# Performance work log

Hardware: AMD Instinct MI355X
Metric: run time of the kernel (lower is better)

Reference implementation:

```python
import jax, jax.numpy as jnp
import numpy as np

E = 1024
H = 16
D = E // H  # head dim 64
B = 2
S = 2048


def setup_inputs() -> dict:
    key = jax.random.key(0)
    k1, k2, k3, k4, k5 = jax.random.split(key, 5)
    scale = 1.0 / np.sqrt(E)
    return {
        "x": jax.random.normal(k1, (B, S, E), dtype=jnp.float32),
        "W_in": jax.random.normal(k2, (E, 3 * E), dtype=jnp.float32) * scale,
        "b_in": jnp.zeros((3 * E,), dtype=jnp.float32),
        "W_out": jax.random.normal(k3, (E, E), dtype=jnp.float32) * scale,
        "b_out": jnp.zeros((E,), dtype=jnp.float32),
        "causal_mask": 1,
    }


def reference(x, W_in, b_in, W_out, b_out, causal_mask):
    b, s, e = x.shape
    qkv = x @ W_in + b_in                      # [B,S,3E]
    q, k, v = jnp.split(qkv, 3, axis=-1)
    # [B,S,E] -> [B,H,S,D]
    q = q.reshape(b, s, H, D).transpose(0, 2, 1, 3)
    k = k.reshape(b, s, H, D).transpose(0, 2, 1, 3)
    v = v.reshape(b, s, H, D).transpose(0, 2, 1, 3)
    scores = jnp.einsum("bhqd,bhkd->bhqk", q, k)
    if causal_mask:
        # mask applied before scaling in the original; -inf is scale-invariant
        mask = jnp.triu(jnp.ones((s, s), dtype=bool), k=1)
        scores = jnp.where(mask, -jnp.inf, scores)
    scores = scores / np.sqrt(D)
    weight = jax.nn.softmax(scores, axis=-1)
    out = jnp.einsum("bhqk,bhkd->bhqd", weight, v)   # [B,H,S,D]
    out = out.transpose(0, 2, 1, 3).reshape(b, s, e)
    return out @ W_out + b_out
```

## Files before the change

### kernel.cpp

```cpp
#include <hip/hip_runtime.h>
#include <hip/hip_bf16.h>
#include <cmath>

typedef __bf16 bf16;
typedef __attribute__((ext_vector_type(8))) __bf16 bf16x8;
typedef __attribute__((ext_vector_type(4))) __bf16 bf16x4;
typedef __attribute__((ext_vector_type(4))) float f32x4;
typedef __attribute__((ext_vector_type(16))) float f32x16;
typedef unsigned int u32;

constexpr int S  = 2048;
constexpr int E  = 1024;
constexpr int H  = 16;
constexpr int D  = 64;
constexpr int B  = 2;
constexpr int M  = B * S;
constexpr int N3 = 3 * E;
constexpr int NROWS = B * H * S;

__constant__ int P_tab_d[16] = {1,1,1,1,1,2,2,2,2,2,2,3,3,3,3,3};
__constant__ int S_tab_d[16] = {0,1,2,3,4,5,7,9,11,13,15,17,20,23,26,29};
__constant__ int c_ord_d[32] = {15,15,10,10, 15,14,14,14,13,9,9,4,
                                13,13,12,12,8,8, 12,11,11,11,7,7,3,
                                6,6, 5,5,2, 1, 0};
__constant__ int p_ord_d[32] = {1,2,0,1, 0,0,1,2,2,0,1,0,
                                0,1,1,2,0,1, 0,0,1,2,0,1,0,
                                0,1, 0,1,0, 0, 0};

static __device__ __forceinline__ void gload16(const void* g, void* l) {
  __builtin_amdgcn_global_load_lds((const __attribute__((address_space(1))) void*)g,
                                   (__attribute__((address_space(3))) void*)l, 16, 0, 0);
}

static __device__ __forceinline__ u32 pack2(float a, float b) {
  union { bf16 h[2]; u32 u; } r;
  r.h[0] = (bf16)a; r.h[1] = (bf16)b;
  return r.u;
}
typedef union { u32 w[4]; bf16x8 v; } FU;

__global__ void k_cvt(const float* __restrict__ in, bf16* __restrict__ out) {
  const int i = (blockIdx.x * blockDim.x + threadIdx.x) * 4;
  const float4 v = *(const float4*)(in + i);
  bf16x4 o = { (bf16)v.x, (bf16)v.y, (bf16)v.z, (bf16)v.w };
  *(bf16x4*)(out + i) = o;
}

__global__ void k_transpose_cvt(const float* __restrict__ in, bf16* __restrict__ out,
                                int R, int C) {
  __shared__ float t[32][33];
  const int c0 = blockIdx.x * 32, r0 = blockIdx.y * 32;
  const int tx = threadIdx.x, ty = threadIdx.y;
  #pragma unroll
  for (int j = 0; j < 32; j += 8)
    t[ty + j][tx] = in[(size_t)(r0 + ty + j) * C + c0 + tx];
  __syncthreads();
  #pragma unroll
  for (int j = 0; j < 32; j += 8)
    out[(size_t)(c0 + ty + j) * R + r0 + tx] = (bf16)t[tx][ty + j];
}

template<int EPI>
__global__ __launch_bounds__(256) void k_gemm(
    const bf16* __restrict__ A, const bf16* __restrict__ Bt,
    const float* __restrict__ bias, float* __restrict__ outF,
    bf16* __restrict__ oQ, bf16* __restrict__ oK, bf16* __restrict__ oV,
    int Kdim, int Nn)
{
  __shared__ __align__(16) char smem[65536];
  const int tid = threadIdx.x;
  const int lane = tid & 63, w = tid >> 6;
  const int lane15 = lane & 15, quad = lane >> 4;
  const int wm = w >> 1, wn = w & 1;

  const int nbx = Nn >> 7;
  const int nwg = gridDim.x;
  const int bid = blockIdx.x;
  const int swz = (bid & 7) * (nwg >> 3) + (bid >> 3);
  const int bn0 = (swz % nbx) * 128;
  const int bm0 = (swz / nbx) * 128;

  const int so0 = w * 1024 + lane * 16;
  int srow[4], slk[4];
  #pragma unroll
  for (int p = 0; p < 4; ++p) {
    const int o = p * 4096 + so0;
    const int row = o >> 7, cbyte = o & 127;
    srow[p] = row;
    slk[p] = (cbyte ^ ((row & 7) << 4)) >> 1;
  }

  f32x4 acc[4][4] = {};
  const int nkt = Kdim >> 6;

  #pragma unroll
  for (int p = 0; p < 4; ++p) {
    gload16(A  + (size_t)(bm0 + srow[p]) * Kdim + slk[p], smem +         p * 4096 + w * 1024);
    gload16(Bt + (size_t)(bn0 + srow[p]) * Kdim + slk[p], smem + 32768 + p * 4096 + w * 1024);
  }

  #pragma unroll 1
  for (int kt = 0; kt < nkt; ++kt) {
    const int cur = kt & 1;
    __builtin_amdgcn_s_barrier();
    if (kt + 1 < nkt) {
      const int k0 = (kt + 1) << 6;
      const int nb = (cur ^ 1) * 16384;
      #pragma unroll
      for (int p = 0; p < 4; ++p) {
        gload16(A  + (size_t)(bm0 + srow[p]) * Kdim + k0 + slk[p],
                smem + nb +         p * 4096 + w * 1024);
        gload16(Bt + (size_t)(bn0 + srow[p]) * Kdim + k0 + slk[p],
                smem + nb + 32768 + p * 4096 + w * 1024);
      }
      asm volatile("s_waitcnt vmcnt(8)" ::: "memory");
    } else {
      asm volatile("s_waitcnt vmcnt(0)" ::: "memory");
    }
    __builtin_amdgcn_s_barrier();

    const char* cA = smem + cur * 16384;
    const char* cB = smem + 32768 + cur * 16384;
    #pragma unroll
    for (int kk = 0; kk < 2; ++kk) {
      bf16x8 af[4], bfr[4];
      #pragma unroll
      for (int f = 0; f < 4; ++f) {
        const int ra = wm * 64 + f * 16 + lane15;
        af[f] = *(const bf16x8*)(cA + ra * 128 +
                 ((kk * 64 + (quad << 4)) ^ ((ra & 7) << 4)));
        const int rb = wn * 64 + f * 16 + lane15;
        bfr[f] = *(const bf16x8*)(cB + rb * 128 +
                 ((kk * 64 + (quad << 4)) ^ ((rb & 7) << 4)));
      }
      #pragma unroll
      for (int i = 0; i < 4; ++i)
        #pragma unroll
        for (int j = 0; j < 4; ++j)
          acc[i][j] = __builtin_amdgcn_mfma_f32_16x16x32_bf16(af[i], bfr[j], acc[i][j], 0, 0, 0);
    }
  }

  if constexpr (EPI == 1) {
    #pragma unroll
    for (int i = 0; i < 4; ++i)
      #pragma unroll
      for (int j = 0; j < 4; ++j) {
        const int n = bn0 + wn * 64 + j * 16 + lane15;
        const float bv = bias[n];
        #pragma unroll
        for (int r = 0; r < 4; ++r) {
          const int m = bm0 + wm * 64 + i * 16 + quad * 4 + r;
          outF[(size_t)m * E + n] = acc[i][j][r] + bv;
        }
      }
  } else {
    const int which = bn0 >> 10;
    const int b  = bm0 >> 11;
    const int s0 = bm0 & (S - 1);
    const int cn0 = bn0 & (E - 1);
    if (which < 2) {
      __builtin_amdgcn_s_barrier();
      char* lC = smem;
      #pragma unroll
      for (int j = 0; j < 4; ++j) {
        const int n_loc = wn * 64 + j * 16 + lane15;
        const float bv = bias[bn0 + n_loc];
        #pragma unroll
        for (int i = 0; i < 4; ++i)
          #pragma unroll
          for (int r = 0; r < 4; ++r) {
            const int m_loc = wm * 64 + i * 16 + quad * 4 + r;
            *(bf16*)(lC + m_loc * 256 + ((n_loc * 2) ^ ((m_loc & 7) << 4))) =
                (bf16)(acc[i][j][r] + bv);
          }
      }
      __builtin_amdgcn_s_barrier();
      const int h0 = cn0 >> 6;
      #pragma unroll
      for (int it = 0; it < 8; ++it) {
        const int cch = w * 64 + it * 8 + (lane >> 3);
        const int m_loc = cch >> 1, hh = cch & 1, piece = lane & 7;
        const bf16x8 vv = *(const bf16x8*)(lC + m_loc * 256 +
                          ((hh * 128 + piece * 16) ^ ((m_loc & 7) << 4)));
        if (which == 0) {
          *(bf16x8*)(oQ + ((size_t)(b * H + h0 + hh) * S + s0 + m_loc) * D + piece * 8) = vv;
        } else {
          const size_t hb = (size_t)(b * H + h0 + hh) * S * D;
          const int tile = (s0 + m_loc) >> 6;
          const int row = m_loc & 63;
          *(bf16x8*)(oK + hb + (size_t)tile * 4096 + (piece >> 1) * 1024 +
                     (row >> 5) * 512 + (32 * (piece & 1) + (row & 31)) * 8) = vv;
        }
      }
    } else {
      #pragma unroll
      for (int j = 0; j < 4; ++j) {
        const int n_loc = wn * 64 + j * 16 + lane15;
        const int cn = cn0 + n_loc;
        const int hv = cn >> 6, dd = cn & 63;
        const float bv = bias[bn0 + n_loc];
        const size_t hb = (size_t)(b * H + hv) * S * D;
        #pragma unroll
        for (int i = 0; i < 4; ++i) {
          const int scol_g = s0 + wm * 64 + i * 16 + quad * 4;
          const int vtile = scol_g >> 6;
          const int cg = (scol_g & 63) >> 3;
          bf16x4 pk = { (bf16)(acc[i][j][0] + bv), (bf16)(acc[i][j][1] + bv),
                        (bf16)(acc[i][j][2] + bv), (bf16)(acc[i][j][3] + bv) };
          *(bf16x4*)(oV + hb + (size_t)vtile * 4096 + (cg >> 1) * 1024 +
                     (dd >> 5) * 512 + (32 * (cg & 1) + (dd & 31)) * 8 +
                     (quad & 1) * 4) = pk;
        }
      }
    }
  }
}

__global__ __launch_bounds__(256, 4) void k_attn(
    const bf16* __restrict__ Qb, const bf16* __restrict__ Kf, const bf16* __restrict__ Vf,
    bf16* __restrict__ pO0, bf16* __restrict__ pO1,
    float* __restrict__ pM, float* __restrict__ pL, const int* __restrict__ cmask)
{
  __shared__ float corr_lds[4][32];
  __shared__ float lrow_lds[4][32];

  const int tid = threadIdx.x, lane = tid & 63, w = tid >> 6;
  const int h = lane >> 5, q31 = lane & 31;
  const int bh = blockIdx.x;
  const int yy = blockIdx.y;
  const int c  = c_ord_d[yy];
  const int p  = p_ord_d[yy];
  const int Pc = P_tab_d[c];
  const int sslot = S_tab_d[c] + p;
  const int causal = cmask[0];
  const float S2 = 0.18033688011112042f;

  const bf16* Qh = Qb + (size_t)bh * S * D;
  const bf16* Kh = Kf + (size_t)bh * S * D;
  const bf16* Vh = Vf + (size_t)bh * S * D;

  const int nt = causal ? (2 * c + 2) : (S / 64);
  const int t0 = (p * nt) / Pc;
  const int t1 = ((p + 1) * nt) / Pc;
  const int q0w = c * 128 + 32 * w;
  const int qg  = q0w + q31;
  const int t1w = causal ? min(t1, ((q0w + 31) >> 6) + 1) : t1;

  bf16x8 qf[4];
  #pragma unroll
  for (int ds = 0; ds < 4; ++ds)
    qf[ds] = *(const bf16x8*)(Qh + (size_t)qg * D + 16 * ds + 8 * h);

  f32x16 o0 = {}, o1 = {};
  float mrun = -INFINITY, lr = 0.f;

  #pragma unroll 1
  for (int t = t0; t < t1w; ++t) {
    const bf16* ktb = Kh + (size_t)t * 4096;
    const bf16* vtb = Vh + (size_t)t * 4096;

    bf16x8 kf0[4], kf1[4];
    #pragma unroll
    for (int ds = 0; ds < 4; ++ds) {
      kf0[ds] = *(const bf16x8*)(ktb + ds * 1024 +       lane * 8);
      kf1[ds] = *(const bf16x8*)(ktb + ds * 1024 + 512 + lane * 8);
    }

    f32x16 s0v = {}, s1v = {};
    __builtin_amdgcn_s_setprio(1);
    #pragma unroll
    for (int ds = 0; ds < 4; ++ds) {
      s0v = __builtin_amdgcn_mfma_f32_32x32x16_bf16(kf0[ds], qf[ds], s0v, 0, 0, 0);
      s1v = __builtin_amdgcn_mfma_f32_32x32x16_bf16(kf1[ds], qf[ds], s1v, 0, 0, 0);
    }
    __builtin_amdgcn_s_setprio(0);

    if (causal && (64 * t + 63 > q0w)) {
      #pragma unroll
      for (int rr = 0; rr < 16; ++rr) {
        const int kg = 64 * t + (rr & 3) + 8 * (rr >> 2) + 4 * h;
        if (kg > qg)      s0v[rr] = -INFINITY;
        if (kg + 32 > qg) s1v[rr] = -INFINITY;
      }
    }

    float a8[8];
    #pragma unroll
    for (int i = 0; i < 8; ++i)
      a8[i] = fmaxf(fmaxf(s0v[i], s0v[i + 8]), fmaxf(s1v[i], s1v[i + 8]));
    float tmax = fmaxf(fmaxf(fmaxf(a8[0], a8[1]), fmaxf(a8[2], a8[3])),
                       fmaxf(fmaxf(a8[4], a8[5]), fmaxf(a8[6], a8[7])));
    tmax = fmaxf(tmax, __shfl_xor(tmax, 32, 64));

    const bool nogrow = __all(tmax <= mrun);
    const float mnew = nogrow ? mrun : fmaxf(mrun, tmax);
    float corrf = 1.f;
    if (!nogrow) {
      corrf = __builtin_amdgcn_exp2f((mrun - mnew) * S2);
      corr_lds[w][q31] = corrf;
    }
    const float msc = mnew * S2;

    #pragma unroll
    for (int rr = 0; rr < 16; ++rr) {
      s0v[rr] = __builtin_amdgcn_exp2f(__builtin_fmaf(s0v[rr], S2, -msc));
      s1v[rr] = __builtin_amdgcn_exp2f(__builtin_fmaf(s1v[rr], S2, -msc));
    }

    float b8[8];
    #pragma unroll
    for (int i = 0; i < 8; ++i)
      b8[i] = (s0v[i] + s0v[i + 8]) + (s1v[i] + s1v[i + 8]);
    float psum = ((b8[0] + b8[1]) + (b8[2] + b8[3])) + ((b8[4] + b8[5]) + (b8[6] + b8[7]));
    psum += __shfl_xor(psum, 32, 64);
    lr = lr * corrf + psum;
    mrun = mnew;

    u32 pk[8][2];
    #pragma unroll
    for (int jj = 0; jj < 4; ++jj) {
      pk[jj][0]     = pack2(s0v[4 * jj],     s0v[4 * jj + 1]);
      pk[jj][1]     = pack2(s0v[4 * jj + 2], s0v[4 * jj + 3]);
      pk[jj + 4][0] = pack2(s1v[4 * jj],     s1v[4 * jj + 1]);
      pk[jj + 4][1] = pack2(s1v[4 * jj + 2], s1v[4 * jj + 3]);
    }

    if (!nogrow) {
      #pragma unroll
      for (int j = 0; j < 4; ++j) {
        const f32x4 cv = *(const f32x4*)&corr_lds[w][8 * j + 4 * h];
        #pragma unroll
        for (int sr = 0; sr < 4; ++sr) {
          o0[4 * j + sr] *= cv[sr];
          o1[4 * j + sr] *= cv[sr];
        }
      }
    }

    __builtin_amdgcn_s_setprio(1);
    #pragma unroll
    for (int ks = 0; ks < 4; ++ks) {
      u32 a0 = pk[2 * ks][0], b0 = pk[2 * ks + 1][0];
      u32 a1 = pk[2 * ks][1], b1 = pk[2 * ks + 1][1];
      asm volatile("v_permlane32_swap_b32 %0, %1" : "+v"(a0), "+v"(b0));
      asm volatile("v_permlane32_swap_b32 %0, %1" : "+v"(a1), "+v"(b1));
      FU f; f.w[0] = a0; f.w[1] = a1; f.w[2] = b0; f.w[3] = b1;
      const bf16x8 vf0 = *(const bf16x8*)(vtb + ks * 1024 +       lane * 8);
      const bf16x8 vf1 = *(const bf16x8*)(vtb + ks * 1024 + 512 + lane * 8);
      o0 = __builtin_amdgcn_mfma_f32_32x32x16_bf16(f.v, vf0, o0, 0, 0, 0);
      o1 = __builtin_amdgcn_mfma_f32_32x32x16_bf16(f.v, vf1, o1, 0, 0, 0);
    }
    __builtin_amdgcn_s_setprio(0);
  }

  const int slotbase = ((bh & 15) * 32 + sslot) * 128;
  if (h == 0) {
    pM[(size_t)(bh * 32 + sslot) * 128 + 32 * w + q31] = mrun;
    pL[(size_t)(bh * 32 + sslot) * 128 + 32 * w + q31] = lr;
  }
  lrow_lds[w][q31] = lr;
  bf16* po = (bh < 16 ? pO0 : pO1) + (size_t)slotbase * D;
  #pragma unroll
  for (int j = 0; j < 4; ++j) {
    const f32x4 lv = *(const f32x4*)&lrow_lds[w][8 * j + 4 * h];
    #pragma unroll
    for (int sr = 0; sr < 4; ++sr) {
      const int rr = 4 * j + sr;
      const float inv = lv[sr] > 0.f ? 1.0f / lv[sr] : 0.f;
      const int qloc = 32 * w + (rr & 3) + 8 * (rr >> 2) + 4 * h;
      bf16* dst = po + (size_t)qloc * D;
      dst[q31]      = (bf16)(o0[rr] * inv);
      dst[32 + q31] = (bf16)(o1[rr] * inv);
    }
  }
}

__global__ __launch_bounds__(256) void k_combine(
    const bf16* __restrict__ pO0, const bf16* __restrict__ pO1,
    const float* __restrict__ pM, const float* __restrict__ pL,
    bf16* __restrict__ AO)
{
  const float S2 = 0.18033688011112042f;
  const int idx = blockIdx.x * 256 + threadIdx.x;
  const int row = idx >> 3, d0 = (idx & 7) * 8;
  const int bh = row >> 11, s = row & 2047;
  const int c = s >> 7, local = s & 127;
  const int Pc = P_tab_d[c], Sc = S_tab_d[c];
  const bf16* pbase = (bh < 16 ? pO0 : pO1);

  float mv[3], lv[3];
  float m = -INFINITY;
  #pragma unroll
  for (int p = 0; p < 3; ++p) {
    if (p < Pc) {
      mv[p] = pM[(size_t)(bh * 32 + Sc + p) * 128 + local];
      lv[p] = pL[(size_t)(bh * 32 + Sc + p) * 128 + local];
      m = fmaxf(m, mv[p]);
    }
  }
  float wsum = 0.f, wv[3];
  #pragma unroll
  for (int p = 0; p < 3; ++p) {
    wv[p] = 0.f;
    if (p < Pc && lv[p] > 0.f) {
      wv[p] = lv[p] * __builtin_amdgcn_exp2f((mv[p] - m) * S2);
      wsum += wv[p];
    }
  }
  const float inv = 1.0f / wsum;
  float acc[8] = {};
  #pragma unroll
  for (int p = 0; p < 3; ++p) {
    if (p < Pc) {
      const bf16x8 a = *(const bf16x8*)(pbase +
          ((size_t)((bh & 15) * 32 + Sc + p) * 128 + local) * D + d0);
      #pragma unroll
      for (int i = 0; i < 8; ++i)
        acc[i] += wv[p] * (float)a[i];
    }
  }
  bf16x8 o;
  #pragma unroll
  for (int i = 0; i < 8; ++i)
    o[i] = (bf16)(acc[i] * inv);
  const int bb = row >> 15, hh = (row >> 11) & 15;
  *(bf16x8*)(AO + ((size_t)(bb * S + s)) * E + hh * D + d0) = o;
}

extern "C" void kernel_launch(void* const* d_in, const int* in_sizes, int n_in,
                              void* d_out, int out_size, void* d_ws, size_t ws_size,
                              hipStream_t stream) {
  (void)in_sizes; (void)n_in; (void)out_size; (void)ws_size;
  const float* x     = (const float*)d_in[0];
  const float* W_in  = (const float*)d_in[1];
  const float* b_in  = (const float*)d_in[2];
  const float* W_out = (const float*)d_in[3];
  const float* b_out = (const float*)d_in[4];
  const int*   cmask = (const int*)d_in[5];

  char* ws = (char*)d_ws;
  bf16* xb    = (bf16*)ws; ws += (size_t)M * E * 2;
  bf16* wtin  = (bf16*)ws; ws += (size_t)N3 * E * 2;
  bf16* wtout = (bf16*)ws; ws += (size_t)E * E * 2;
  bf16* qB    = (bf16*)ws; ws += (size_t)B * H * S * D * 2;
  bf16* kF    = (bf16*)ws; ws += (size_t)B * H * S * D * 2;
  bf16* vF    = (bf16*)ws; ws += (size_t)B * H * S * D * 2;
  bf16* ao    = (bf16*)ws; ws += (size_t)M * E * 2;
  bf16* pO1   = (bf16*)ws; ws += (size_t)NROWS * D * 2;
  float* pMb  = (float*)ws; ws += (size_t)2 * NROWS * 4;
  float* pLb  = (float*)ws; ws += (size_t)2 * NROWS * 4;
  bf16* pO0   = xb;

  k_cvt<<<M * E / 1024, 256, 0, stream>>>(x, xb);
  k_transpose_cvt<<<dim3(N3 / 32, E / 32), dim3(32, 8), 0, stream>>>(W_in, wtin, E, N3);
  k_transpose_cvt<<<dim3(E / 32, E / 32), dim3(32, 8), 0, stream>>>(W_out, wtout, E, E);
  k_gemm<0><<<dim3((M / 128) * (N3 / 128)), 256, 0, stream>>>(
      xb, wtin, b_in, nullptr, qB, kF, vF, E, N3);
  k_attn<<<dim3(32, 32), 256, 0, stream>>>(qB, kF, vF, pO0, pO1, pMb, pLb, cmask);
  k_combine<<<NROWS * 8 / 256, 256, 0, stream>>>(pO0, pO1, pMb, pLb, ao);
  k_gemm<1><<<dim3((M / 128) * (E / 128)), 256, 0, stream>>>(
      ao, wtout, b_out, (float*)d_out, nullptr, nullptr, nullptr, E, E);
}
```

Baseline: 108.8 us.

## Fuse prep conversions into one launch and software-pipeline K/V loads in attention

Merges the x conversion and both weight transpose-converts into a single k_prep kernel, removing two launches and their gaps. In the attention loop, the K fragments for the next tile are prefetched into registers while the current tile is processed, and the V fragments are loaded right after QK^T rather than inside the PV loop. The occupancy hint of 4 waves in k_attn is dropped so the compiler can use the extra registers this prefetching needs, which may lower occupancy.

```diff
diff --git a/kernel.cpp b/kernel.cpp
--- a/kernel.cpp
+++ b/kernel.cpp
@@ -39,25 +39,41 @@
 }
 typedef union { u32 w[4]; bf16x8 v; } FU;
 
-__global__ void k_cvt(const float* __restrict__ in, bf16* __restrict__ out) {
-  const int i = (blockIdx.x * blockDim.x + threadIdx.x) * 4;
-  const float4 v = *(const float4*)(in + i);
-  bf16x4 o = { (bf16)v.x, (bf16)v.y, (bf16)v.z, (bf16)v.w };
-  *(bf16x4*)(out + i) = o;
-}
-
-__global__ void k_transpose_cvt(const float* __restrict__ in, bf16* __restrict__ out,
-                                int R, int C) {
-  __shared__ float t[32][33];
-  const int c0 = blockIdx.x * 32, r0 = blockIdx.y * 32;
-  const int tx = threadIdx.x, ty = threadIdx.y;
-  #pragma unroll
-  for (int j = 0; j < 32; j += 8)
-    t[ty + j][tx] = in[(size_t)(r0 + ty + j) * C + c0 + tx];
-  __syncthreads();
-  #pragma unroll
-  for (int j = 0; j < 32; j += 8)
-    out[(size_t)(c0 + ty + j) * R + r0 + tx] = (bf16)t[tx][ty + j];
+__global__ __launch_bounds__(256) void k_prep(
+    const float* __restrict__ x, bf16* __restrict__ xb,
+    const float* __restrict__ W_in, bf16* __restrict__ wtin,
+    const float* __restrict__ W_out, bf16* __restrict__ wtout)
+{
+  const int bid = blockIdx.x;
+  if (bid < 4096) {
+    const int i = (bid * 256 + threadIdx.x) * 4;
+    const float4 v = *(const float4*)(x + i);
+    bf16x4 o = { (bf16)v.x, (bf16)v.y, (bf16)v.z, (bf16)v.w };
+    *(bf16x4*)(xb + i) = o;
+  } else {
+    __shared__ float t[32][33];
+    const float* in;
+    bf16* out;
+    int R, C, bx, by;
+    if (bid < 4096 + 3072) {
+      const int b = bid - 4096;
+      in = W_in; out = wtin; R = E; C = N3;
+      bx = b % (N3 / 32); by = b / (N3 / 32);
+    } else {
+      const int b = bid - 4096 - 3072;
+      in = W_out; out = wtout; R = E; C = E;
+      bx = b % (E / 32); by = b / (E / 32);
+    }
+    const int c0 = bx * 32, r0 = by * 32;
+    const int tx = threadIdx.x & 31, ty = threadIdx.x >> 5;
+    #pragma unroll
+    for (int j = 0; j < 32; j += 8)
+      t[ty + j][tx] = in[(size_t)(r0 + ty + j) * C + c0 + tx];
+    __syncthreads();
+    #pragma unroll
+    for (int j = 0; j < 32; j += 8)
+      out[(size_t)(c0 + ty + j) * R + r0 + tx] = (bf16)t[tx][ty + j];
+  }
 }
 
 template<int EPI>
@@ -217,7 +233,7 @@
   }
 }
 
-__global__ __launch_bounds__(256, 4) void k_attn(
+__global__ __launch_bounds__(256) void k_attn(
     const bf16* __restrict__ Qb, const bf16* __restrict__ Kf, const bf16* __restrict__ Vf,
     bf16* __restrict__ pO0, bf16* __restrict__ pO1,
     float* __restrict__ pM, float* __restrict__ pL, const int* __restrict__ cmask)
@@ -255,26 +271,43 @@
   f32x16 o0 = {}, o1 = {};
   float mrun = -INFINITY, lr = 0.f;
 
+  bf16x8 kc0[4], kc1[4];
+  {
+    const bf16* ktb = Kh + (size_t)t0 * 4096;
+    #pragma unroll
+    for (int ds = 0; ds < 4; ++ds) {
+      kc0[ds] = *(const bf16x8*)(ktb + ds * 1024 +       lane * 8);
+      kc1[ds] = *(const bf16x8*)(ktb + ds * 1024 + 512 + lane * 8);
+    }
+  }
+
   #pragma unroll 1
   for (int t = t0; t < t1w; ++t) {
-    const bf16* ktb = Kh + (size_t)t * 4096;
     const bf16* vtb = Vh + (size_t)t * 4096;
-
-    bf16x8 kf0[4], kf1[4];
-    #pragma unroll
-    for (int ds = 0; ds < 4; ++ds) {
-      kf0[ds] = *(const bf16x8*)(ktb + ds * 1024 +       lane * 8);
-      kf1[ds] = *(const bf16x8*)(ktb + ds * 1024 + 512 + lane * 8);
-    }
 
     f32x16 s0v = {}, s1v = {};
     __builtin_amdgcn_s_setprio(1);
     #pragma unroll
     for (int ds = 0; ds < 4; ++ds) {
-      s0v = __builtin_amdgcn_mfma_f32_32x32x16_bf16(kf0[ds], qf[ds], s0v, 0, 0, 0);
-      s1v = __builtin_amdgcn_mfma_f32_32x32x16_bf16(kf1[ds], qf[ds], s1v, 0, 0, 0);
+      s0v = __builtin_amdgcn_mfma_f32_32x32x16_bf16(kc0[ds], qf[ds], s0v, 0, 0, 0);
+      s1v = __builtin_amdgcn_mfma_f32_32x32x16_bf16(kc1[ds], qf[ds], s1v, 0, 0, 0);
     }
     __builtin_amdgcn_s_setprio(0);
+
+    bf16x8 vf0[4], vf1[4];
+    #pragma unroll
+    for (int ks = 0; ks < 4; ++ks) {
+      vf0[ks] = *(const bf16x8*)(vtb + ks * 1024 +       lane * 8);
+      vf1[ks] = *(const bf16x8*)(vtb + ks * 1024 + 512 + lane * 8);
+    }
+    if (t + 1 < t1w) {
+      const bf16* ktb2 = Kh + (size_t)(t + 1) * 4096;
+      #pragma unroll
+      for (int ds = 0; ds < 4; ++ds) {
+        kc0[ds] = *(const bf16x8*)(ktb2 + ds * 1024 +       lane * 8);
+        kc1[ds] = *(const bf16x8*)(ktb2 + ds * 1024 + 512 + lane * 8);
+      }
+    }
 
     if (causal && (64 * t + 63 > q0w)) {
       #pragma unroll
@@ -346,10 +379,8 @@
       asm volatile("v_permlane32_swap_b32 %0, %1" : "+v"(a0), "+v"(b0));
       asm volatile("v_permlane32_swap_b32 %0, %1" : "+v"(a1), "+v"(b1));
       FU f; f.w[0] = a0; f.w[1] = a1; f.w[2] = b0; f.w[3] = b1;
-      const bf16x8 vf0 = *(const bf16x8*)(vtb + ks * 1024 +       lane * 8);
-      const bf16x8 vf1 = *(const bf16x8*)(vtb + ks * 1024 + 512 + lane * 8);
-      o0 = __builtin_amdgcn_mfma_f32_32x32x16_bf16(f.v, vf0, o0, 0, 0, 0);
-      o1 = __builtin_amdgcn_mfma_f32_32x32x16_bf16(f.v, vf1, o1, 0, 0, 0);
+      o0 = __builtin_amdgcn_mfma_f32_32x32x16_bf16(f.v, vf0[ks], o0, 0, 0, 0);
+      o1 = __builtin_amdgcn_mfma_f32_32x32x16_bf16(f.v, vf1[ks], o1, 0, 0, 0);
     }
     __builtin_amdgcn_s_setprio(0);
   }
@@ -452,9 +483,7 @@
   float* pLb  = (float*)ws; ws += (size_t)2 * NROWS * 4;
   bf16* pO0   = xb;
 
-  k_cvt<<<M * E / 1024, 256, 0, stream>>>(x, xb);
-  k_transpose_cvt<<<dim3(N3 / 32, E / 32), dim3(32, 8), 0, stream>>>(W_in, wtin, E, N3);
-  k_transpose_cvt<<<dim3(E / 32, E / 32), dim3(32, 8), 0, stream>>>(W_out, wtout, E, E);
+  k_prep<<<4096 + 3072 + 1024, 256, 0, stream>>>(x, xb, W_in, wtin, W_out, wtout);
   k_gemm<0><<<dim3((M / 128) * (N3 / 128)), 256, 0, stream>>>(
       xb, wtin, b_in, nullptr, qB, kF, vF, E, N3);
   k_attn<<<dim3(32, 32), 256, 0, stream>>>(qB, kF, vF, pO0, pO1, pMb, pLb, cmask);
```

Result: no change. 110.4 us (+1.5%).
